# Kernel optimization log

Hardware: AMD Instinct MI355X
Metric: run time of the kernel (lower is better)

The kernel has to match this reference:

```python
import jax, jax.numpy as jnp
import numpy as np

B, S, D = 2, 1024, 5120
NH, NKV, HD = 80, 8, 128
GROUPS = NH // NKV
SCALE = HD ** -0.5
ROPE_THETA = 1.0e7


def setup_inputs() -> dict:
    key = jax.random.key(0)
    ks = jax.random.split(key, 8)
    hidden_states = jax.random.normal(ks[0], (B, S, D), dtype=jnp.float32)
    # real RoPE tables from rope_theta (default rope_type)
    inv_freq = 1.0 / (ROPE_THETA ** (np.arange(0, HD, 2, dtype=np.float32) / HD))  # [HD/2]
    pos = np.arange(S, dtype=np.float32)
    freqs = np.outer(pos, inv_freq)                      # [S, HD/2]
    emb = np.concatenate([freqs, freqs], axis=-1)        # [S, HD]
    cos = jnp.asarray(np.broadcast_to(np.cos(emb), (B, S, HD)).copy())
    sin = jnp.asarray(np.broadcast_to(np.sin(emb), (B, S, HD)).copy())
    w_scale = 0.02
    q_w = jax.random.normal(ks[1], (NH * HD, D), dtype=jnp.float32) * w_scale
    q_b = jax.random.normal(ks[2], (NH * HD,), dtype=jnp.float32) * w_scale
    k_w = jax.random.normal(ks[3], (NKV * HD, D), dtype=jnp.float32) * w_scale
    k_b = jax.random.normal(ks[4], (NKV * HD,), dtype=jnp.float32) * w_scale
    v_w = jax.random.normal(ks[5], (NKV * HD, D), dtype=jnp.float32) * w_scale
    v_b = jax.random.normal(ks[6], (NKV * HD,), dtype=jnp.float32) * w_scale
    o_w = jax.random.normal(ks[7], (D, NH * HD), dtype=jnp.float32) * w_scale
    return dict(hidden_states=hidden_states, cos=cos, sin=sin,
                q_w=q_w, q_b=q_b, k_w=k_w, k_b=k_b, v_w=v_w, v_b=v_b, o_w=o_w)


def _rotate_half(x):
    x1, x2 = jnp.split(x, 2, axis=-1)
    return jnp.concatenate([-x2, x1], axis=-1)


def reference(hidden_states, cos, sin, q_w, q_b, k_w, k_b, v_w, v_b, o_w):
    b, s, _ = hidden_states.shape
    # QKV projections (bias on q/k/v per attention_bias=True)
    q = (hidden_states @ q_w.T + q_b).reshape(b, s, NH, HD).transpose(0, 2, 1, 3)   # [b,NH,s,hd]
    k = (hidden_states @ k_w.T + k_b).reshape(b, s, NKV, HD).transpose(0, 2, 1, 3)  # [b,NKV,s,hd]
    v = (hidden_states @ v_w.T + v_b).reshape(b, s, NKV, HD).transpose(0, 2, 1, 3)
    # RoPE (rotate_half form); cos/sin broadcast over head dim
    c = cos[:, None, :, :]
    sn = sin[:, None, :, :]
    q = q * c + _rotate_half(q) * sn
    k = k * c + _rotate_half(k) * sn
    # GQA: repeat kv heads to match query heads
    k = jnp.repeat(k, GROUPS, axis=1)  # [b,NH,s,hd]
    v = jnp.repeat(v, GROUPS, axis=1)
    scores = jnp.einsum('bhqd,bhkd->bhqk', q, k) * SCALE
    causal = jnp.tril(jnp.ones((s, s), dtype=bool))
    scores = jnp.where(causal[None, None], scores, jnp.finfo(scores.dtype).min)
    attn = jax.nn.softmax(scores, axis=-1)
    out = jnp.einsum('bhqk,bhkd->bhqd', attn, v)                 # [b,NH,s,hd]
    out = out.transpose(0, 2, 1, 3).reshape(b, s, NH * HD)
    return out @ o_w.T                                           # o_proj, no bias
```

## Files before the change

### kernel.cpp

```cpp
#include <hip/hip_runtime.h>
#include <hip/hip_bf16.h>

#define NH 80
#define NKV 8
#define HD 128
#define GROUPS 10
#define SEQ 1024
#define BATCH 2
#define DMODEL 5120
#define NQKV 12288
#define MROWS 2048
#define QCOLS 10240
#define KOFF 10240
#define VOFF 11264
#define ATTN_SCALE 0.08838834764831845f

typedef __attribute__((ext_vector_type(8))) __bf16 bf16x8;
typedef __attribute__((ext_vector_type(4))) float f32x4;

__device__ inline unsigned short f2bf(float f) {
  unsigned u = __float_as_uint(f);
  u = (u + 0x7fffu + ((u >> 16) & 1u)) >> 16;
  return (unsigned short)u;
}
__device__ inline float bf2f(unsigned short h) {
  return __uint_as_float(((unsigned)h) << 16);
}

template <typename T>
__device__ inline T ld_vec(const void* p) {
  T v;
  __builtin_memcpy(&v, p, sizeof(T));
  return v;
}

__device__ inline void gload_lds16(const void* g, void* l) {
  __builtin_amdgcn_global_load_lds(
      (const __attribute__((address_space(1))) void*)g,
      (__attribute__((address_space(3))) void*)l, 16, 0, 0);
}

__global__ __launch_bounds__(256) void cvt_f32_bf16(
    const float* __restrict__ src, unsigned short* __restrict__ dst, long n) {
  long i = ((long)blockIdx.x * 256 + threadIdx.x) * 8;
  if (i + 8 > n) return;
  float4 a = *reinterpret_cast<const float4*>(src + i);
  float4 b = *reinterpret_cast<const float4*>(src + i + 4);
  union { unsigned short u[8]; uint4 v; } r;
  r.u[0] = f2bf(a.x); r.u[1] = f2bf(a.y); r.u[2] = f2bf(a.z); r.u[3] = f2bf(a.w);
  r.u[4] = f2bf(b.x); r.u[5] = f2bf(b.y); r.u[6] = f2bf(b.z); r.u[7] = f2bf(b.w);
  *reinterpret_cast<uint4*>(dst + i) = r.v;
}

__global__ __launch_bounds__(256) void concat_bias(
    const float* __restrict__ qb, const float* __restrict__ kb,
    const float* __restrict__ vb, float* __restrict__ out) {
  int i = blockIdx.x * 256 + threadIdx.x;
  if (i >= NQKV) return;
  float v;
  if (i < KOFF) v = qb[i];
  else if (i < VOFF) v = kb[i - KOFF];
  else v = vb[i - VOFF];
  out[i] = v;
}

template <int OUT_BF16, int HAS_BIAS>
__global__ __launch_bounds__(256, 2) void gemm_bt64(
    const unsigned short* __restrict__ A, const unsigned short* __restrict__ W,
    const float* __restrict__ bias, void* __restrict__ Cout,
    int M, int N, int K) {
  __shared__ unsigned short As[128 * 64];
  __shared__ unsigned short Bs[128 * 64];
  const int t = threadIdx.x;
  const int lane = t & 63, wave = t >> 6;
  const int m0 = blockIdx.y * 128, n0 = blockIdx.x * 128;
  const int wr = (wave >> 1) * 64, wc = (wave & 1) * 64;
  const int lr = lane & 15, lg = lane >> 4;
  int st_row[4], st_col[4];
#pragma unroll
  for (int ch = 0; ch < 4; ++ch) {
    int ol = wave * 1024 + ch * 4096 + lane * 16;
    int row = ol >> 7, cb = ol & 127;
    st_row[ch] = row;
    st_col[ch] = cb ^ ((row & 7) << 4);
  }
  f32x4 acc[4][4] = {};
  const int swz = (lr & 7) << 4;
  for (int k0 = 0; k0 < K; k0 += 64) {
#pragma unroll
    for (int ch = 0; ch < 4; ++ch) {
      int od = wave * 1024 + ch * 4096;
      gload_lds16((const char*)A +
                      ((size_t)(m0 + st_row[ch]) * K + k0) * 2 + st_col[ch],
                  (char*)As + od);
      gload_lds16((const char*)W +
                      ((size_t)(n0 + st_row[ch]) * K + k0) * 2 + st_col[ch],
                  (char*)Bs + od);
    }
    __syncthreads();
    bf16x8 af[4][2], bfr[4][2];
#pragma unroll
    for (int ks = 0; ks < 2; ++ks) {
      int colb = (ks * 64 + lg * 16) ^ swz;
#pragma unroll
      for (int m = 0; m < 4; ++m)
        af[m][ks] =
            ld_vec<bf16x8>((const char*)As + (wr + m * 16 + lr) * 128 + colb);
#pragma unroll
      for (int n = 0; n < 4; ++n)
        bfr[n][ks] =
            ld_vec<bf16x8>((const char*)Bs + (wc + n * 16 + lr) * 128 + colb);
    }
#pragma unroll
    for (int ks = 0; ks < 2; ++ks)
#pragma unroll
      for (int m = 0; m < 4; ++m)
#pragma unroll
        for (int n = 0; n < 4; ++n)
          acc[m][n] = __builtin_amdgcn_mfma_f32_16x16x32_bf16(
              af[m][ks], bfr[n][ks], acc[m][n], 0, 0, 0);
    __syncthreads();
  }
#pragma unroll
  for (int n = 0; n < 4; ++n) {
    int col = n0 + wc + n * 16 + lr;
    float bv = HAS_BIAS ? bias[col] : 0.0f;
#pragma unroll
    for (int m = 0; m < 4; ++m) {
#pragma unroll
      for (int r = 0; r < 4; ++r) {
        int row = m0 + wr + m * 16 + lg * 4 + r;
        float v = acc[m][n][r] + bv;
        if (OUT_BF16)
          ((unsigned short*)Cout)[(size_t)row * N + col] = f2bf(v);
        else
          ((float*)Cout)[(size_t)row * N + col] = v;
      }
    }
  }
}

__global__ __launch_bounds__(256) void rope_kernel(
    unsigned short* __restrict__ qkv, const float* __restrict__ cs,
    const float* __restrict__ sn) {
  int idx = blockIdx.x * 256 + threadIdx.x;
  int quad = idx & 15;
  int rest = idx >> 4;
  int slot = rest % 88;
  int row = rest / 88;
  if (row >= MROWS) return;
  int col = slot < NH ? slot * HD : KOFF + (slot - NH) * HD;
  unsigned short* p = qkv + (size_t)row * NQKV + col;
  const float* cp = cs + (size_t)row * HD;
  const float* sp = sn + (size_t)row * HD;
  int d0 = quad * 4;
  float4 c1 = *reinterpret_cast<const float4*>(cp + d0);
  float4 s1 = *reinterpret_cast<const float4*>(sp + d0);
  float4 c2 = *reinterpret_cast<const float4*>(cp + d0 + 64);
  float4 s2 = *reinterpret_cast<const float4*>(sp + d0 + 64);
  ushort4 x1 = *reinterpret_cast<const ushort4*>(p + d0);
  ushort4 x2 = *reinterpret_cast<const ushort4*>(p + d0 + 64);
  ushort4 o1, o2;
  float a, b;
  a = bf2f(x1.x); b = bf2f(x2.x);
  o1.x = f2bf(a * c1.x - b * s1.x); o2.x = f2bf(b * c2.x + a * s2.x);
  a = bf2f(x1.y); b = bf2f(x2.y);
  o1.y = f2bf(a * c1.y - b * s1.y); o2.y = f2bf(b * c2.y + a * s2.y);
  a = bf2f(x1.z); b = bf2f(x2.z);
  o1.z = f2bf(a * c1.z - b * s1.z); o2.z = f2bf(b * c2.z + a * s2.z);
  a = bf2f(x1.w); b = bf2f(x2.w);
  o1.w = f2bf(a * c1.w - b * s1.w); o2.w = f2bf(b * c2.w + a * s2.w);
  *reinterpret_cast<ushort4*>(p + d0) = o1;
  *reinterpret_cast<ushort4*>(p + d0 + 64) = o2;
}

__global__ __launch_bounds__(256, 2) void attn_kernel(
    const unsigned short* __restrict__ qkv, unsigned short* __restrict__ out) {
  __shared__ unsigned short Ks[64][136];
  __shared__ unsigned short Vt[128][64];
  __shared__ unsigned short Ps[4][32][72];
  const int t = threadIdx.x, lane = t & 63, wave = t >> 6;
  const int lr = lane & 15, lg = lane >> 4;
  const int blk = blockIdx.x;
  const int qt = blk & 7;
  const int bh = blk >> 3;
  const int h = bh % NH, b = bh / NH;
  const int kvh = h / GROUPS;
  const int q0 = qt * 128;
  const int wrow0 = q0 + wave * 32;
  const unsigned short* Qb = qkv + (size_t)(b * SEQ) * NQKV + h * HD;
  const unsigned short* Kb = qkv + (size_t)(b * SEQ) * NQKV + KOFF + kvh * HD;
  const unsigned short* Vb = qkv + (size_t)(b * SEQ) * NQKV + VOFF + kvh * HD;
  bf16x8 qf[2][4];
#pragma unroll
  for (int rb = 0; rb < 2; ++rb)
#pragma unroll
    for (int kk = 0; kk < 4; ++kk)
      qf[rb][kk] = ld_vec<bf16x8>(Qb + (size_t)(wrow0 + rb * 16 + lr) * NQKV +
                                  kk * 32 + lg * 8);
  f32x4 acc[2][8] = {};
  float mrow[2][4], lrow[2][4];
#pragma unroll
  for (int rb = 0; rb < 2; ++rb)
#pragma unroll
    for (int r = 0; r < 4; ++r) { mrow[rb][r] = -__builtin_inff(); lrow[rb][r] = 0.f; }

  const int ntile = (q0 + 128) >> 6;
  for (int tt = 0; tt < ntile; ++tt) {
    const int kv0 = tt * 64;
    __syncthreads();
#pragma unroll
    for (int i = 0; i < 4; ++i) {
      int e = i * 2048 + t * 8;
      int row = e >> 7, colc = e & 127;
      uint4 dk = ld_vec<uint4>(Kb + (size_t)(kv0 + row) * NQKV + colc);
      *reinterpret_cast<uint4*>(&Ks[row][colc]) = dk;
      uint4 dv = ld_vec<uint4>(Vb + (size_t)(kv0 + row) * NQKV + colc);
      const unsigned short* pv = reinterpret_cast<const unsigned short*>(&dv);
#pragma unroll
      for (int j = 0; j < 8; ++j) {
        int dd = colc + j;
        int gp = ((row >> 3) + dd + (dd >> 3)) & 7;
        Vt[dd][(gp << 3) | (row & 7)] = pv[j];
      }
    }
    __syncthreads();
    if (kv0 > wrow0 + 31) continue;
    const bool needMask = (kv0 + 63) > wrow0;
#pragma unroll
    for (int rb = 0; rb < 2; ++rb) {
      f32x4 sf[4] = {};
#pragma unroll
      for (int kk = 0; kk < 4; ++kk) {
#pragma unroll
        for (int cb = 0; cb < 4; ++cb) {
          bf16x8 kfr = ld_vec<bf16x8>(&Ks[cb * 16 + lr][kk * 32 + lg * 8]);
          sf[cb] = __builtin_amdgcn_mfma_f32_16x16x32_bf16(qf[rb][kk], kfr,
                                                           sf[cb], 0, 0, 0);
        }
      }
#pragma unroll
      for (int r = 0; r < 4; ++r) {
        int qrow = wrow0 + rb * 16 + lg * 4 + r;
        float mx = -3.0e38f;
#pragma unroll
        for (int cb = 0; cb < 4; ++cb) {
          float s = sf[cb][r] * ATTN_SCALE;
          if (needMask && (kv0 + cb * 16 + lr) > qrow) s = -__builtin_inff();
          sf[cb][r] = s;
          mx = fmaxf(mx, s);
        }
        mx = fmaxf(mx, __shfl_xor(mx, 1));
        mx = fmaxf(mx, __shfl_xor(mx, 2));
        mx = fmaxf(mx, __shfl_xor(mx, 4));
        mx = fmaxf(mx, __shfl_xor(mx, 8));
        float mold = mrow[rb][r];
        float mnew = fmaxf(mold, mx);
        float sfac = __expf(mold - mnew);
        mrow[rb][r] = mnew;
        float ps = 0.f;
#pragma unroll
        for (int cb = 0; cb < 4; ++cb) {
          float p = __expf(sf[cb][r] - mnew);
          ps += p;
          Ps[wave][rb * 16 + lg * 4 + r][cb * 16 + lr] = f2bf(p);
        }
        ps += __shfl_xor(ps, 1);
        ps += __shfl_xor(ps, 2);
        ps += __shfl_xor(ps, 4);
        ps += __shfl_xor(ps, 8);
        lrow[rb][r] = lrow[rb][r] * sfac + ps;
#pragma unroll
        for (int n = 0; n < 8; ++n) acc[rb][n][r] *= sfac;
      }
    }
#pragma unroll
    for (int kk = 0; kk < 2; ++kk) {
      bf16x8 vf[8];
#pragma unroll
      for (int cb = 0; cb < 8; ++cb) {
        int dd = cb * 16 + lr;
        int gp = (kk * 4 + lg + dd + (dd >> 3)) & 7;
        vf[cb] = ld_vec<bf16x8>(&Vt[dd][gp << 3]);
      }
#pragma unroll
      for (int rb = 0; rb < 2; ++rb) {
        bf16x8 pa = ld_vec<bf16x8>(&Ps[wave][rb * 16 + lr][kk * 32 + lg * 8]);
#pragma unroll
        for (int cb = 0; cb < 8; ++cb)
          acc[rb][cb] = __builtin_amdgcn_mfma_f32_16x16x32_bf16(pa, vf[cb],
                                                                acc[rb][cb], 0, 0, 0);
      }
    }
  }
#pragma unroll
  for (int rb = 0; rb < 2; ++rb)
#pragma unroll
    for (int n = 0; n < 8; ++n)
#pragma unroll
      for (int r = 0; r < 4; ++r) {
        int qrow = wrow0 + rb * 16 + lg * 4 + r;
        float v = acc[rb][n][r] / lrow[rb][r];
        out[(size_t)(b * SEQ + qrow) * QCOLS + h * HD + n * 16 + lr] = f2bf(v);
      }
}

extern "C" void kernel_launch(void* const* d_in, const int* in_sizes, int n_in,
                              void* d_out, int out_size, void* d_ws,
                              size_t ws_size, hipStream_t stream) {
  const float* hs   = (const float*)d_in[0];
  const float* cosb = (const float*)d_in[1];
  const float* sinb = (const float*)d_in[2];
  const float* q_w  = (const float*)d_in[3];
  const float* q_b  = (const float*)d_in[4];
  const float* k_w  = (const float*)d_in[5];
  const float* k_b  = (const float*)d_in[6];
  const float* v_w  = (const float*)d_in[7];
  const float* v_b  = (const float*)d_in[8];
  const float* o_w  = (const float*)d_in[9];

  char* ws = (char*)d_ws;
  unsigned short* hsB  = (unsigned short*)(ws);
  unsigned short* wqkv = (unsigned short*)(ws + 20971520ll);
  unsigned short* wo   = (unsigned short*)(ws + 146800640ll);
  unsigned short* qkv  = (unsigned short*)(ws + 251658240ll);
  unsigned short* attn = (unsigned short*)(ws + 301989888ll);
  float* bqkv          = (float*)(ws + 343932928ll);

  cvt_f32_bf16<<<dim3(5120), dim3(256), 0, stream>>>(hs, hsB, (long)MROWS * DMODEL);
  cvt_f32_bf16<<<dim3(25600), dim3(256), 0, stream>>>(q_w, wqkv, (long)QCOLS * DMODEL);
  cvt_f32_bf16<<<dim3(2560), dim3(256), 0, stream>>>(
      k_w, wqkv + (size_t)KOFF * DMODEL, (long)1024 * DMODEL);
  cvt_f32_bf16<<<dim3(2560), dim3(256), 0, stream>>>(
      v_w, wqkv + (size_t)VOFF * DMODEL, (long)1024 * DMODEL);
  cvt_f32_bf16<<<dim3(25600), dim3(256), 0, stream>>>(o_w, wo, (long)5120 * 10240);
  concat_bias<<<dim3(48), dim3(256), 0, stream>>>(q_b, k_b, v_b, bqkv);

  gemm_bt64<1, 1><<<dim3(96, 16), dim3(256), 0, stream>>>(
      hsB, wqkv, bqkv, qkv, MROWS, NQKV, DMODEL);
  rope_kernel<<<dim3(11264), dim3(256), 0, stream>>>(qkv, cosb, sinb);
  attn_kernel<<<dim3(1280), dim3(256), 0, stream>>>(qkv, attn);
  gemm_bt64<0, 0><<<dim3(40, 16), dim3(256), 0, stream>>>(
      attn, wo, nullptr, d_out, MROWS, 5120, 10240);
}
```

Measured before the change: 898.8 us.

## Double-buffer LDS in QKV GEMM to overlap global loads with MFMA

```diff
diff --git a/kernel.cpp b/kernel.cpp
--- a/kernel.cpp
+++ b/kernel.cpp
@@ -62,6 +62,98 @@
   else if (i < VOFF) v = kb[i - KOFF];
   else v = vb[i - VOFF];
   out[i] = v;
+}
+
+template <int OUT_BF16, int HAS_BIAS>
+__global__ __launch_bounds__(256, 2) void gemm_t3(
+    const unsigned short* __restrict__ A, const unsigned short* __restrict__ W,
+    const float* __restrict__ bias, void* __restrict__ Cout,
+    int M, int N, int K) {
+  __shared__ unsigned short As[2][128 * 64];
+  __shared__ unsigned short Bs[2][128 * 64];
+  const int t = threadIdx.x;
+  const int lane = t & 63, wave = t >> 6;
+  const int m0 = blockIdx.y * 128, n0 = blockIdx.x * 128;
+  const int wr = (wave >> 1) * 64, wc = (wave & 1) * 64;
+  const int lr = lane & 15, lg = lane >> 4;
+  int st_row[4], st_col[4];
+#pragma unroll
+  for (int ch = 0; ch < 4; ++ch) {
+    int ol = wave * 1024 + ch * 4096 + lane * 16;
+    int row = ol >> 7, cb = ol & 127;
+    st_row[ch] = row;
+    st_col[ch] = cb ^ ((row & 7) << 4);
+  }
+  f32x4 acc[4][4] = {};
+  const int swz = (lr & 7) << 4;
+  auto STAGE = [&](int buf, int k0) {
+#pragma unroll
+    for (int ch = 0; ch < 4; ++ch) {
+      int od = wave * 1024 + ch * 4096;
+      gload_lds16((const char*)A +
+                      ((size_t)(m0 + st_row[ch]) * K + k0) * 2 + st_col[ch],
+                  (char*)&As[buf][0] + od);
+      gload_lds16((const char*)W +
+                      ((size_t)(n0 + st_row[ch]) * K + k0) * 2 + st_col[ch],
+                  (char*)&Bs[buf][0] + od);
+    }
+  };
+  auto COMPUTE = [&](int buf) {
+    bf16x8 af[4][2], bfr[4][2];
+#pragma unroll
+    for (int ks = 0; ks < 2; ++ks) {
+      int colb = (ks * 64 + lg * 16) ^ swz;
+#pragma unroll
+      for (int m = 0; m < 4; ++m)
+        af[m][ks] = ld_vec<bf16x8>((const char*)&As[buf][0] +
+                                   (wr + m * 16 + lr) * 128 + colb);
+#pragma unroll
+      for (int n = 0; n < 4; ++n)
+        bfr[n][ks] = ld_vec<bf16x8>((const char*)&Bs[buf][0] +
+                                    (wc + n * 16 + lr) * 128 + colb);
+    }
+#pragma unroll
+    for (int ks = 0; ks < 2; ++ks)
+#pragma unroll
+      for (int m = 0; m < 4; ++m)
+#pragma unroll
+        for (int n = 0; n < 4; ++n)
+          acc[m][n] = __builtin_amdgcn_mfma_f32_16x16x32_bf16(
+              af[m][ks], bfr[n][ks], acc[m][n], 0, 0, 0);
+  };
+  auto FENCE = [&]() {
+    asm volatile("s_waitcnt vmcnt(0)" ::: "memory");
+    __builtin_amdgcn_s_barrier();
+    __builtin_amdgcn_sched_barrier(0);
+  };
+
+  STAGE(0, 0);
+  __syncthreads();
+  for (int k0 = 0; k0 < K; k0 += 128) {
+    STAGE(1, k0 + 64);
+    COMPUTE(0);
+    FENCE();
+    if (k0 + 128 < K) STAGE(0, k0 + 128);
+    COMPUTE(1);
+    FENCE();
+  }
+#pragma unroll
+  for (int n = 0; n < 4; ++n) {
+    int col = n0 + wc + n * 16 + lr;
+    float bv = HAS_BIAS ? bias[col] : 0.0f;
+#pragma unroll
+    for (int m = 0; m < 4; ++m) {
+#pragma unroll
+      for (int r = 0; r < 4; ++r) {
+        int row = m0 + wr + m * 16 + lg * 4 + r;
+        float v = acc[m][n][r] + bv;
+        if (OUT_BF16)
+          ((unsigned short*)Cout)[(size_t)row * N + col] = f2bf(v);
+        else
+          ((float*)Cout)[(size_t)row * N + col] = v;
+      }
+    }
+  }
 }
 
 template <int OUT_BF16, int HAS_BIAS>
@@ -336,7 +428,7 @@
   cvt_f32_bf16<<<dim3(25600), dim3(256), 0, stream>>>(o_w, wo, (long)5120 * 10240);
   concat_bias<<<dim3(48), dim3(256), 0, stream>>>(q_b, k_b, v_b, bqkv);
 
-  gemm_bt64<1, 1><<<dim3(96, 16), dim3(256), 0, stream>>>(
+  gemm_t3<1, 1><<<dim3(96, 16), dim3(256), 0, stream>>>(
       hsB, wqkv, bqkv, qkv, MROWS, NQKV, DMODEL);
   rope_kernel<<<dim3(11264), dim3(256), 0, stream>>>(qkv, cosb, sinb);
   attn_kernel<<<dim3(1280), dim3(256), 0, stream>>>(qkv, attn);
```

Measured after the change: 980.3 us. 1.09x slower.

## Write V transposed from QKV GEMM epilogue to avoid in-attention transpose

Applied to the files above, without the earlier changes.

```diff
diff --git a/kernel.cpp b/kernel.cpp
--- a/kernel.cpp
+++ b/kernel.cpp
@@ -64,11 +64,11 @@
   out[i] = v;
 }
 
-template <int OUT_BF16, int HAS_BIAS>
+template <int OUT_BF16, int HAS_BIAS, int WRITE_VT>
 __global__ __launch_bounds__(256, 2) void gemm_bt64(
     const unsigned short* __restrict__ A, const unsigned short* __restrict__ W,
     const float* __restrict__ bias, void* __restrict__ Cout,
-    int M, int N, int K) {
+    unsigned short* __restrict__ vT, int M, int N, int K) {
   __shared__ unsigned short As[128 * 64];
   __shared__ unsigned short Bs[128 * 64];
   const int t = threadIdx.x;
@@ -131,10 +131,17 @@
       for (int r = 0; r < 4; ++r) {
         int row = m0 + wr + m * 16 + lg * 4 + r;
         float v = acc[m][n][r] + bv;
-        if (OUT_BF16)
-          ((unsigned short*)Cout)[(size_t)row * N + col] = f2bf(v);
-        else
+        if (OUT_BF16) {
+          if (WRITE_VT && col >= VOFF) {
+            int vcol = col - VOFF;
+            int bb = row >> 10, ss = row & 1023;
+            vT[((size_t)(bb * 1024 + vcol)) * SEQ + ss] = f2bf(v);
+          } else {
+            ((unsigned short*)Cout)[(size_t)row * N + col] = f2bf(v);
+          }
+        } else {
           ((float*)Cout)[(size_t)row * N + col] = v;
+        }
       }
     }
   }
@@ -175,9 +182,10 @@
 }
 
 __global__ __launch_bounds__(256, 2) void attn_kernel(
-    const unsigned short* __restrict__ qkv, unsigned short* __restrict__ out) {
+    const unsigned short* __restrict__ qkv, const unsigned short* __restrict__ vT,
+    unsigned short* __restrict__ out) {
   __shared__ unsigned short Ks[64][136];
-  __shared__ unsigned short Vt[128][64];
+  __shared__ unsigned short Vs[128][64];
   __shared__ unsigned short Ps[4][32][72];
   const int t = threadIdx.x, lane = t & 63, wave = t >> 6;
   const int lr = lane & 15, lg = lane >> 4;
@@ -190,7 +198,7 @@
   const int wrow0 = q0 + wave * 32;
   const unsigned short* Qb = qkv + (size_t)(b * SEQ) * NQKV + h * HD;
   const unsigned short* Kb = qkv + (size_t)(b * SEQ) * NQKV + KOFF + kvh * HD;
-  const unsigned short* Vb = qkv + (size_t)(b * SEQ) * NQKV + VOFF + kvh * HD;
+  const unsigned short* Vtb = vT + ((size_t)(b * 1024 + kvh * HD)) * SEQ;
   bf16x8 qf[2][4];
 #pragma unroll
   for (int rb = 0; rb < 2; ++rb)
@@ -212,17 +220,13 @@
 #pragma unroll
     for (int i = 0; i < 4; ++i) {
       int e = i * 2048 + t * 8;
-      int row = e >> 7, colc = e & 127;
-      uint4 dk = ld_vec<uint4>(Kb + (size_t)(kv0 + row) * NQKV + colc);
-      *reinterpret_cast<uint4*>(&Ks[row][colc]) = dk;
-      uint4 dv = ld_vec<uint4>(Vb + (size_t)(kv0 + row) * NQKV + colc);
-      const unsigned short* pv = reinterpret_cast<const unsigned short*>(&dv);
-#pragma unroll
-      for (int j = 0; j < 8; ++j) {
-        int dd = colc + j;
-        int gp = ((row >> 3) + dd + (dd >> 3)) & 7;
-        Vt[dd][(gp << 3) | (row & 7)] = pv[j];
-      }
+      int krow = e >> 7, kcol = e & 127;
+      uint4 dk = ld_vec<uint4>(Kb + (size_t)(kv0 + krow) * NQKV + kcol);
+      *reinterpret_cast<uint4*>(&Ks[krow][kcol]) = dk;
+      int d = e >> 6, kc = e & 63;
+      uint4 dv = ld_vec<uint4>(Vtb + (size_t)d * SEQ + kv0 + kc);
+      *reinterpret_cast<uint4*>((char*)&Vs[0][0] + d * 128 +
+                                ((kc * 2) ^ ((d & 7) << 4))) = dv;
     }
     __syncthreads();
     if (kv0 > wrow0 + 31) continue;
@@ -280,8 +284,8 @@
 #pragma unroll
       for (int cb = 0; cb < 8; ++cb) {
         int dd = cb * 16 + lr;
-        int gp = (kk * 4 + lg + dd + (dd >> 3)) & 7;
-        vf[cb] = ld_vec<bf16x8>(&Vt[dd][gp << 3]);
+        vf[cb] = ld_vec<bf16x8>((const char*)&Vs[0][0] + dd * 128 +
+                                ((kk * 64 + lg * 16) ^ ((lr & 7) << 4)));
       }
 #pragma unroll
       for (int rb = 0; rb < 2; ++rb) {
@@ -326,6 +330,7 @@
   unsigned short* qkv  = (unsigned short*)(ws + 251658240ll);
   unsigned short* attn = (unsigned short*)(ws + 301989888ll);
   float* bqkv          = (float*)(ws + 343932928ll);
+  unsigned short* vT   = (unsigned short*)(ws + 343982080ll);
 
   cvt_f32_bf16<<<dim3(5120), dim3(256), 0, stream>>>(hs, hsB, (long)MROWS * DMODEL);
   cvt_f32_bf16<<<dim3(25600), dim3(256), 0, stream>>>(q_w, wqkv, (long)QCOLS * DMODEL);
@@ -336,10 +341,10 @@
   cvt_f32_bf16<<<dim3(25600), dim3(256), 0, stream>>>(o_w, wo, (long)5120 * 10240);
   concat_bias<<<dim3(48), dim3(256), 0, stream>>>(q_b, k_b, v_b, bqkv);
 
-  gemm_bt64<1, 1><<<dim3(96, 16), dim3(256), 0, stream>>>(
-      hsB, wqkv, bqkv, qkv, MROWS, NQKV, DMODEL);
+  gemm_bt64<1, 1, 1><<<dim3(96, 16), dim3(256), 0, stream>>>(
+      hsB, wqkv, bqkv, qkv, vT, MROWS, NQKV, DMODEL);
   rope_kernel<<<dim3(11264), dim3(256), 0, stream>>>(qkv, cosb, sinb);
-  attn_kernel<<<dim3(1280), dim3(256), 0, stream>>>(qkv, attn);
-  gemm_bt64<0, 0><<<dim3(40, 16), dim3(256), 0, stream>>>(
-      attn, wo, nullptr, d_out, MROWS, 5120, 10240);
-}
+  attn_kernel<<<dim3(1280), dim3(256), 0, stream>>>(qkv, vT, attn);
+  gemm_bt64<0, 0, 0><<<dim3(40, 16), dim3(256), 0, stream>>>(
+      attn, wo, nullptr, d_out, nullptr, MROWS, 5120, 10240);
+}
```

Measured after the change: 980.1 us. 1.09x slower.
